# Performance work log

Measured on AMD Instinct MI355X. Metric: run time of the kernel, lower is better.

The kernel has to match this reference:

```python
import jax, jax.numpy as jnp
import numpy as np

TEMP_LEN = 16
TARGET_LEN = 22
DIM = 768
HEADS = 12
B = 16
NT = TEMP_LEN * TEMP_LEN          # 256 template tokens
NG = TARGET_LEN * TARGET_LEN      # 484 target tokens
N = NT + NG                       # 740
POS_HID = 512


def _gaussian_heatmap(center, size, sig=1.0):
    x_axis = np.linspace(0, size[0] - 1, size[0]) - center[0]
    y_axis = np.linspace(0, size[1] - 1, size[1]) - center[1]
    xx, yy = np.meshgrid(x_axis, y_axis)
    return np.exp(-0.5 * (xx ** 2 + yy ** 2) / sig ** 2)


def _bias_index(L):
    # faithful to getBiasIndex (w_len == h_len here)
    coords = np.stack(np.meshgrid(np.arange(L), np.arange(L), indexing='ij'))  # [2,L,L]
    flat = coords.reshape(2, -1)                                               # [2,L*L]
    rel = (flat[:, :, None] - flat[:, None, :]).transpose(1, 2, 0).astype(np.int64)
    rel[:, :, 0] += L - 1
    rel[:, :, 1] += L - 1
    rel[:, :, 0] *= 2 * L - 1
    return rel.sum(-1)  # [L*L, L*L]


def setup_inputs() -> dict:
    key = jax.random.key(0)
    ks = jax.random.split(key, 12)
    f32 = jnp.float32
    x = jax.random.normal(ks[0], (B, N, DIM), dtype=f32)
    temp_q = jax.random.normal(ks[1], (B, NT, DIM), dtype=f32)
    target_q = jax.random.normal(ks[2], (B, NG, DIM), dtype=f32)
    # linear weights stored [in, out] (transposed torch layout)
    w = lambda k, i, o: jax.random.normal(k, (i, o), dtype=f32) * 0.02
    q_w = w(ks[3], DIM, DIM)
    k_w = w(ks[4], DIM, DIM)
    v_w = w(ks[5], DIM, DIM)
    proj_w = w(ks[6], DIM, DIM)
    proj_b = jnp.zeros((DIM,), dtype=f32)
    rpb_table = jax.random.normal(ks[7], ((2 * TARGET_LEN - 1) ** 2, HEADS), dtype=f32) * 0.0002
    rpb_table_temp = jax.random.normal(ks[8], ((2 * TEMP_LEN - 1) ** 2, HEADS), dtype=f32) * 0.0002
    pos_w1 = w(ks[9], 2, POS_HID)
    pos_b1 = jnp.zeros((POS_HID,), dtype=f32)
    pos_w2 = w(ks[10], POS_HID, HEADS)
    pos_b2 = jnp.zeros((HEADS,), dtype=f32)
    # deterministic cross-bias coordinate table (non-learned buffer)
    temp_tab = _gaussian_heatmap((TEMP_LEN // 2, TEMP_LEN // 2), (TEMP_LEN, TEMP_LEN)).astype(np.float32).flatten() \
        + np.linspace(-0.2, 0.2, NT, dtype=np.float32)
    targ_tab = _gaussian_heatmap((TARGET_LEN // 2, TARGET_LEN // 2), (TARGET_LEN, TARGET_LEN)).astype(np.float32).flatten() \
        + np.linspace(-0.2, 0.2, NG, dtype=np.float32)
    # torch.meshgrid default indexing='ij': [2, NT, NG] -> permute(1,2,0) -> [NT,NG,2]
    temp_target = np.stack(np.meshgrid(temp_tab, targ_tab, indexing='ij')).transpose(1, 2, 0)
    target_temp_tab = jnp.asarray(temp_target.transpose(1, 0, 2))  # [NG, NT, 2]
    temp_idx = jnp.asarray(_bias_index(TEMP_LEN))       # [NT, NT] int64
    target_idx = jnp.asarray(_bias_index(TARGET_LEN))   # [NG, NG] int64
    return {
        'x': x, 'temp_q': temp_q, 'target_q': target_q,
        'q_w': q_w, 'k_w': k_w, 'v_w': v_w, 'proj_w': proj_w, 'proj_b': proj_b,
        'rpb_table': rpb_table, 'rpb_table_temp': rpb_table_temp,
        'pos_w1': pos_w1, 'pos_b1': pos_b1, 'pos_w2': pos_w2, 'pos_b2': pos_b2,
        'target_temp_tab': target_temp_tab,
        'temp_idx': temp_idx, 'target_idx': target_idx,
    }


def reference(x, temp_q, target_q, q_w, k_w, v_w, proj_w, proj_b,
              rpb_table, rpb_table_temp, pos_w1, pos_b1, pos_w2, pos_b2,
              target_temp_tab, temp_idx, target_idx):
    Bsz, Ntok, C = x.shape
    H = HEADS
    hd = C // H
    scale = hd ** -0.5

    q_in = jnp.concatenate([temp_q, target_q], axis=1)                 # [B,N,C]
    q = (q_in @ q_w).reshape(Bsz, Ntok, H, hd).transpose(0, 2, 1, 3)   # [B,H,N,hd]
    k = (x @ k_w).reshape(Bsz, Ntok, H, hd).transpose(0, 2, 1, 3)
    v = (x @ v_w).reshape(Bsz, Ntok, H, hd).transpose(0, 2, 1, 3)

    # gathered relative position biases -> [H, Ni, Ni]
    temp_rpb = rpb_table_temp[temp_idx.reshape(-1)].reshape(NT, NT, H).transpose(2, 0, 1)
    targ_rpb = rpb_table[target_idx.reshape(-1)].reshape(NG, NG, H).transpose(2, 0, 1)
    # MLP cross bias: [NG, NT, 2] -> [NG, NT, H] -> [H, NG, NT]
    hid = jax.nn.relu(target_temp_tab @ pos_w1 + pos_b1)
    target_temp_bias = (hid @ pos_w2 + pos_b2).transpose(2, 0, 1)      # [H,NG,NT]
    temp_target_bias = target_temp_bias.transpose(0, 2, 1)             # [H,NT,NG]
    top = jnp.concatenate([temp_rpb, temp_target_bias], axis=2)        # [H,NT,N]
    bot = jnp.concatenate([target_temp_bias, targ_rpb], axis=2)        # [H,NG,N]
    bias = jnp.concatenate([top, bot], axis=1)[None]                   # [1,H,N,N]

    attn = jnp.einsum('bhnd,bhmd->bhnm', q, k) * scale + bias
    attn = jax.nn.softmax(attn, axis=-1)
    out = jnp.einsum('bhnm,bhmd->bhnd', attn, v).transpose(0, 2, 1, 3).reshape(Bsz, Ntok, C)
    return out @ proj_w + proj_b
```

## Files before the change

### kernel.cpp

```cpp
#include <hip/hip_runtime.h>


typedef unsigned short u16;
typedef short bf16x8 __attribute__((ext_vector_type(8)));
typedef float f32x4 __attribute__((ext_vector_type(4)));

#define BSZ   16
#define NTOK  740
#define NTMP  256
#define NTGT  484
#define DIMC  768
#define NHEAD 12
#define HDIM  64
#define MROWS (BSZ*NTOK)
#define LOG2E 1.44269504f
#define NEGS  (-23.0831032f)

__device__ __forceinline__ float bflo(unsigned int u) {
    return __uint_as_float(u << 16);
}
__device__ __forceinline__ float bfhi(unsigned int u) {
    return __uint_as_float(u & 0xffff0000u);
}
__device__ __forceinline__ u16 f2bf(float f) {
    unsigned int u = __float_as_uint(f);
    u += 0x7fffu + ((u >> 16) & 1u);
    return (u16)(u >> 16);
}

__device__ __forceinline__ void gl_lds16(const u16* g, u16* l) {
    __builtin_amdgcn_global_load_lds(
        (const __attribute__((address_space(1))) unsigned int*)(unsigned long long)g,
        (__attribute__((address_space(3))) unsigned int*)(unsigned int)(unsigned long long)l,
        16, 0, 0);
}

__device__ __forceinline__ size_t b2off(int h, int i, int j) {
    return ((size_t)(h * NTOK + i)) * 768 + ((j >> 6) << 6) + ((j & 15) << 2) + ((j >> 4) & 3);
}

#define PREP_MLP  484
#define PREP_TRW  (PREP_MLP + 576)
#define PREP_ALL  (PREP_TRW + 2220)

__global__ __launch_bounds__(256) void prep_kernel(
    const float* __restrict__ w0, const float* __restrict__ w1,
    const float* __restrict__ w2, const float* __restrict__ w3,
    u16* __restrict__ Wt,
    const float* __restrict__ rpb, const float* __restrict__ rpbt,
    const int* __restrict__ tidx, const int* __restrict__ gidx,
    const float* __restrict__ pw1, const float* __restrict__ pb1,
    const float* __restrict__ pw2, const float* __restrict__ pb2,
    const float* __restrict__ tab, u16* __restrict__ bias)
{
    __shared__ float T[64][65];
    const int blk = blockIdx.x;
    const int tid = threadIdx.x;

    if (blk < PREP_MLP) {
        int g = blk;
        int t = tid;
        float a  = tab[(g * NTMP + t) * 2 + 0];
        float bb = tab[(g * NTMP + t) * 2 + 1];
        float acc[NHEAD];
        #pragma unroll
        for (int h = 0; h < NHEAD; h++) acc[h] = pb2[h];
        for (int k = 0; k < 512; k++) {
            float hid = fmaxf(a * pw1[k] + bb * pw1[512 + k] + pb1[k], 0.0f);
            #pragma unroll
            for (int h = 0; h < NHEAD; h++) acc[h] += hid * pw2[k * NHEAD + h];
        }
        #pragma unroll
        for (int h = 0; h < NHEAD; h++) {
            u16 v = f2bf(acc[h] * LOG2E);
            bias[b2off(h, t, NTMP + g)] = v;
            bias[b2off(h, NTMP + g, t)] = v;
        }
    } else if (blk < PREP_TRW) {
        int t = blk - PREP_MLP;
        int z = t / 144, rem = t - z * 144;
        int bx = rem % 12, by = rem / 12;
        const float* src = (z == 0) ? w0 : (z == 1) ? w1 : (z == 2) ? w2 : w3;
        const float scale = (z == 0) ? 0.125f * LOG2E : 1.0f;
        u16* dst = Wt + (size_t)z * DIMC * DIMC;
        int out0 = bx * 64, in0 = by * 64;
        #pragma unroll
        for (int l = 0; l < 4; l++) {
            int u = tid + (l << 8);
            int r = u >> 4, c4 = (u & 15) << 2;
            float4 p = *(const float4*)(src + (size_t)(in0 + r) * DIMC + out0 + c4);
            T[r][c4] = p.x; T[r][c4 + 1] = p.y; T[r][c4 + 2] = p.z; T[r][c4 + 3] = p.w;
        }
        __syncthreads();
        #pragma unroll
        for (int l = 0; l < 2; l++) {
            int u = tid + (l << 8);
            int r = u >> 3, c8 = (u & 7) << 3;
            u16 e[8];
            #pragma unroll
            for (int i = 0; i < 8; i++) e[i] = f2bf(T[c8 + i][r] * scale);
            *(uint4*)(dst + (size_t)(out0 + r) * DIMC + in0 + c8) = *(uint4*)e;
        }
    } else {
        int t = blk - PREP_TRW;
        int jb = t % 3, i = t / 3;
        int j = jb * 256 + tid;
        u16 vals[NHEAD];
        if (j >= NTOK) {
            u16 neg = f2bf(-1e30f);
            #pragma unroll
            for (int h = 0; h < NHEAD; h++) vals[h] = neg;
        } else if (i < NTMP && j < NTMP) {
            int idx = tidx[i * NTMP + j];
            #pragma unroll
            for (int h = 0; h < NHEAD; h++) vals[h] = f2bf(rpbt[idx * NHEAD + h] * LOG2E);
        } else if (i >= NTMP && j >= NTMP) {
            int idx = gidx[(i - NTMP) * NTGT + (j - NTMP)];
            #pragma unroll
            for (int h = 0; h < NHEAD; h++) vals[h] = f2bf(rpb[idx * NHEAD + h] * LOG2E);
        } else {
            return;
        }
        #pragma unroll
        for (int h = 0; h < NHEAD; h++) bias[b2off(h, i, j)] = vals[h];
    }
}

__global__ __launch_bounds__(256, 4) void gemm_qkv(
    const float* __restrict__ x, const float* __restrict__ tq,
    const float* __restrict__ gq, const u16* __restrict__ Wt,
    u16* __restrict__ Qo, u16* __restrict__ Ko, u16* __restrict__ Vo)
{
    __shared__ __align__(16) u16 As[4096];
    __shared__ __align__(16) u16 Bs[2][8192];
    const int tid = threadIdx.x;
    const int lane = tid & 63, w = tid >> 6;
    const int quad = lane >> 4, ln = lane & 15;

    const int nwg = 18 * 185;
    const int flat = blockIdx.y * 18 + blockIdx.x;
    const int q = nwg >> 3, r = nwg & 7;
    const int xcd = flat & 7, sidx = flat >> 3;
    const int wg = (xcd < r) ? xcd * (q + 1) + sidx
                             : r * (q + 1) + (xcd - r) * q + sidx;
    const int by = wg / 18, bx = wg - by * 18;

    const int m0 = by << 6;
    const int wm = (w >> 1) << 5, wn = (w & 1) << 6;

    const int p = (bx < 6) ? 0 : (bx < 12) ? 1 : 2;
    const int nn = (bx - p * 6) << 7;
    const u16* Wb = Wt + (size_t)p * DIMC * DIMC + (size_t)nn * DIMC;
    u16* Co = (p == 0) ? Qo : (p == 1) ? Ko : Vo;

    const int rr = tid >> 2, qq = tid & 3;
    const int arow = m0 + rr;
    const float* aptr;
    if (p == 0) {
        int b = arow / NTOK, n = arow - b * NTOK;
        aptr = (n < NTMP)
             ? tq + ((size_t)(b * NTMP + n)) * DIMC
             : gq + ((size_t)(b * NTGT + (n - NTMP))) * DIMC;
    } else {
        aptr = x + (size_t)arow * DIMC;
    }
    const int wof0 = ((2 * qq + 0) * 64 + (rr ^ (2 * qq + 0))) * 8;
    const int wof1 = ((2 * qq + 1) * 64 + (rr ^ (2 * qq + 1))) * 8;

    float4 a0, a1, a2, a3;

#define LOADA(t) do {                                                         \
    const float* s_ = aptr + ((t) << 6) + (qq << 4);                          \
    a0 = ((const float4*)s_)[0]; a1 = ((const float4*)s_)[1];                 \
    a2 = ((const float4*)s_)[2]; a3 = ((const float4*)s_)[3];                 \
    } while (0)

#define WRITEA() do {                                                         \
    u16 e_[16] = {f2bf(a0.x), f2bf(a0.y), f2bf(a0.z), f2bf(a0.w),             \
                  f2bf(a1.x), f2bf(a1.y), f2bf(a1.z), f2bf(a1.w),             \
                  f2bf(a2.x), f2bf(a2.y), f2bf(a2.z), f2bf(a2.w),             \
                  f2bf(a3.x), f2bf(a3.y), f2bf(a3.z), f2bf(a3.w)};            \
    *(uint4*)&As[wof0] = ((uint4*)e_)[0];                                     \
    *(uint4*)&As[wof1] = ((uint4*)e_)[1];                                     \
    } while (0)

#define STAGEB(t, s) do {                                                     \
    _Pragma("unroll")                                                         \
    for (int l = 0; l < 4; l++) {                                             \
        int f = tid + (l << 8);                                               \
        int c8 = f >> 7, r2 = f & 127;                                        \
        gl_lds16(Wb + (size_t)r2 * DIMC + ((t) << 6) + c8 * 8, &Bs[s][f * 8]); \
    } } while (0)

    f32x4 acc[2][4];
    #pragma unroll
    for (int i = 0; i < 2; i++)
        #pragma unroll
        for (int j = 0; j < 4; j++) acc[i][j] = (f32x4){0.f, 0.f, 0.f, 0.f};

    LOADA(0);
    STAGEB(0, 0);
    __syncthreads();
    WRITEA();
    __syncthreads();

    int buf = 0;
    #pragma unroll 1
    for (int t = 0; t < 12; t++) {
        if (t < 11) {
            LOADA(t + 1);
            STAGEB(t + 1, buf ^ 1);
        }
        #pragma unroll
        for (int kp = 0; kp < 2; kp++) {
            const int kc0 = (kp << 2) + quad;
            bf16x8 af[2], bfr[4];
            #pragma unroll
            for (int mt = 0; mt < 2; mt++)
                af[mt] = *(const bf16x8*)
                    &As[(kc0 * 64 + ((wm + mt * 16 + ln) ^ kc0)) * 8];
            #pragma unroll
            for (int nt = 0; nt < 4; nt++)
                bfr[nt] = *(const bf16x8*)
                    &Bs[buf][(kc0 * 128 + wn + nt * 16 + ln) * 8];
            #pragma unroll
            for (int mt = 0; mt < 2; mt++)
                #pragma unroll
                for (int nt = 0; nt < 4; nt++)
                    acc[mt][nt] = __builtin_amdgcn_mfma_f32_16x16x32_bf16(
                        af[mt], bfr[nt], acc[mt][nt], 0, 0, 0);
        }
        if (t < 11) {
            __syncthreads();
            WRITEA();
            __syncthreads();
            buf ^= 1;
        }
    }
#undef LOADA
#undef WRITEA
#undef STAGEB

    #pragma unroll
    for (int mt = 0; mt < 2; mt++)
        #pragma unroll
        for (int reg = 0; reg < 4; reg++) {
            int grow = m0 + wm + mt * 16 + (quad << 2) + reg;
            #pragma unroll
            for (int nt = 0; nt < 4; nt++)
                Co[(size_t)grow * DIMC + nn + wn + nt * 16 + ln]
                    = f2bf(acc[mt][nt][reg]);
        }
}

__global__ __launch_bounds__(256) void gemm_proj(
    const u16* __restrict__ A, const u16* __restrict__ Wt,
    const float* __restrict__ pb, float* __restrict__ Cf)
{
    __shared__ __align__(16) u16 As[2][8192];
    __shared__ __align__(16) u16 Bs[2][8192];
    const int tid = threadIdx.x;
    const int lane = tid & 63, w = tid >> 6;
    const int quad = lane >> 4, ln = lane & 15;

    const int nwg = 6 * 93;
    const int flat = blockIdx.y * 6 + blockIdx.x;
    const int q = nwg >> 3, r = nwg & 7;
    const int xcd = flat & 7, sidx = flat >> 3;
    const int wg = (xcd < r) ? xcd * (q + 1) + sidx
                             : r * (q + 1) + (xcd - r) * q + sidx;
    const int by = wg / 6, bx = wg - by * 6;

    const int m0 = by << 7;
    const int wm = (w >> 1) << 6, wn = (w & 1) << 6;
    const int nn = bx << 7;
    const u16* Wb = Wt + (size_t)nn * DIMC;

    f32x4 acc[4][4];
    #pragma unroll
    for (int i = 0; i < 4; i++)
        #pragma unroll
        for (int j = 0; j < 4; j++)
            acc[i][j] = (f32x4){0.f, 0.f, 0.f, 0.f};

#define STAGE(s, k0) do {                                                     \
    _Pragma("unroll")                                                         \
    for (int l = 0; l < 4; l++) {                                             \
        int f = tid + (l << 8);                                  \
        int c8 = f >> 7, rr = f & 127;                                        \
        int grow = m0 + rr; if (grow >= MROWS) grow = MROWS - 1;              \
        gl_lds16(A + (size_t)grow * DIMC + (k0) + c8 * 8, &As[s][f * 8]);     \
        gl_lds16(Wb + (size_t)rr * DIMC + (k0) + c8 * 8, &Bs[s][f * 8]);      \
    } } while (0)

#define COMPUTE(s) do {                                                       \
    _Pragma("unroll")                                                         \
    for (int kp = 0; kp < 2; kp++) {                                          \
        bf16x8 af[4], bfr[4];                                                 \
        _Pragma("unroll")                                                     \
        for (int mt = 0; mt < 4; mt++)                                        \
            af[mt] = *(const bf16x8*)                                         \
                &As[s][(((kp << 2) + quad) * 128 + wm + mt * 16 + ln) * 8];   \
        _Pragma("unroll")                                                     \
        for (int nt = 0; nt < 4; nt++)                                        \
            bfr[nt] = *(const bf16x8*)                                        \
                &Bs[s][(((kp << 2) + quad) * 128 + wn + nt * 16 + ln) * 8];   \
        _Pragma("unroll")                                                     \
        for (int mt = 0; mt < 4; mt++)                                        \
            _Pragma("unroll")                                                 \
            for (int nt = 0; nt < 4; nt++)                                    \
                acc[mt][nt] = __builtin_amdgcn_mfma_f32_16x16x32_bf16(        \
                    af[mt], bfr[nt], acc[mt][nt], 0, 0, 0);                   \
    } } while (0)

    STAGE(0, 0);
    __syncthreads();
    #pragma unroll 1
    for (int t = 0; t < 12; t += 2) {
        STAGE(1, (t + 1) << 6);
        COMPUTE(0);
        __syncthreads();
        if (t < 10) STAGE(0, (t + 2) << 6);
        COMPUTE(1);
        __syncthreads();
    }

#undef STAGE
#undef COMPUTE

    #pragma unroll
    for (int mt = 0; mt < 4; mt++) {
        #pragma unroll
        for (int reg = 0; reg < 4; reg++) {
            int grow = m0 + wm + mt * 16 + (quad << 2) + reg;
            if (grow >= MROWS) continue;
            #pragma unroll
            for (int nt = 0; nt < 4; nt++) {
                int gcol = nn + wn + nt * 16 + ln;
                Cf[(size_t)grow * DIMC + gcol] = acc[mt][nt][reg] + pb[gcol];
            }
        }
    }
}

__global__ __launch_bounds__(256) void attn_mfma(
    const u16* __restrict__ Qg, const u16* __restrict__ Kg,
    const u16* __restrict__ Vg, const u16* __restrict__ bias,
    u16* __restrict__ ctx)
{
    __shared__ __align__(16) u16 KsL[4096];
    __shared__ __align__(16) u16 VtL[64 * 72];
    __shared__ __align__(16) u16 Pw[4][16][72];

    const int tid = threadIdx.x;
    const int lane = tid & 63, w = tid >> 6;
    const int quad = lane >> 4, ln = lane & 15;

    const int flat = (blockIdx.z * 12 + blockIdx.y) * 12 + blockIdx.x;
    const int wg = (flat & 7) * 288 + (flat >> 3);
    const int h = wg / 192;
    const int rem = wg - h * 192;
    const int b = rem / 12;
    const int q0 = (rem - b * 12) << 6;

    const int mbase = q0 + (w << 4);
    const u16* bp = bias + ((size_t)h * NTOK) * 768;

    bf16x8 aq[2];
    {
        int qrow = mbase + ln; if (qrow >= NTOK) qrow = NTOK - 1;
        #pragma unroll
        for (int kp = 0; kp < 2; kp++)
            aq[kp] = *(const bf16x8*)(Qg + ((size_t)(b * NTOK + qrow)) * DIMC
                                      + h * HDIM + kp * 32 + (quad << 3));
    }
    int boff[4];
    #pragma unroll
    for (int reg = 0; reg < 4; reg++) {
        int rr = mbase + (quad << 2) + reg;
        if (rr >= NTOK) rr = NTOK - 1;
        boff[reg] = rr * 768 + (ln << 2);
    }

    const int pswz = ((ln >> 2) & 3) << 4;

    float rs[4] = {};
    f32x4 O[4];
    #pragma unroll
    for (int dt = 0; dt < 4; dt++) O[dt] = (f32x4){0.f, 0.f, 0.f, 0.f};

    for (int j0 = 0; j0 < NTOK; j0 += 64) {
        __syncthreads();
        #pragma unroll
        for (int l = 0; l < 2; l++) {
            int f = tid + (l << 8);
            int chunk = f >> 6, jr = f & 63;
            int krow = j0 + jr; if (krow >= NTOK) krow = NTOK - 1;
            gl_lds16(Kg + ((size_t)(b * NTOK + krow)) * DIMC + h * HDIM + chunk * 8,
                     KsL + f * 8);
        }
        uint2 bvv[4];
        #pragma unroll
        for (int reg = 0; reg < 4; reg++)
            bvv[reg] = *(const uint2*)(bp + boff[reg] + j0);
        #pragma unroll
        for (int l = 0; l < 2; l++) {
            int u = tid + (l << 8);
            int jr = u >> 3, d0 = (u & 7) << 3;
            int vrow = j0 + jr; if (vrow >= NTOK) vrow = NTOK - 1;
            uint4 p = *(const uint4*)(Vg + ((size_t)(b * NTOK + vrow)) * DIMC + h * HDIM + d0);
            const u16* pe = (const u16*)&p;
            int jswz = jr ^ d0;
            #pragma unroll
            for (int i = 0; i < 8; i++) VtL[(d0 + i) * 72 + jswz] = pe[i];
        }
        __syncthreads();

        bf16x8 bv[4][2];
        #pragma unroll
        for (int dt = 0; dt < 4; dt++) {
            int key8 = ((dt * 2 + (ln >> 3)) & 7) << 3;
            #pragma unroll
            for (int kp = 0; kp < 2; kp++) {
                int koff = (kp * 32 + (quad << 3)) ^ key8;
                bv[dt][kp] = *(const bf16x8*)&VtL[(dt * 16 + ln) * 72 + koff];
            }
        }

        f32x4 s[4];
        #pragma unroll
        for (int nt = 0; nt < 4; nt++) s[nt] = (f32x4){NEGS, NEGS, NEGS, NEGS};
        __builtin_amdgcn_s_setprio(1);
        #pragma unroll
        for (int kp = 0; kp < 2; kp++)
            #pragma unroll
            for (int nt = 0; nt < 4; nt++) {
                bf16x8 bk = *(const bf16x8*)
                    &KsL[(((kp << 2) + quad) * 64 + nt * 16 + ln) * 8];
                s[nt] = __builtin_amdgcn_mfma_f32_16x16x32_bf16(aq[kp], bk, s[nt], 0, 0, 0);
            }
        __builtin_amdgcn_s_setprio(0);

        #pragma unroll
        for (int reg = 0; reg < 4; reg++) {
            uint2 bb = bvv[reg];
            float p0 = __builtin_exp2f(s[0][reg] + bflo(bb.x));
            float p1 = __builtin_exp2f(s[1][reg] + bfhi(bb.x));
            float p2 = __builtin_exp2f(s[2][reg] + bflo(bb.y));
            float p3 = __builtin_exp2f(s[3][reg] + bfhi(bb.y));
            s[0][reg] = p0; s[1][reg] = p1;
            s[2][reg] = p2; s[3][reg] = p3;
            rs[reg] += p0 + p1 + p2 + p3;
        }
        u16* pwb = &Pw[w][0][0];
        #pragma unroll
        for (int nt = 0; nt < 4; nt++) {
            int colw = ((nt ^ quad) << 4) + ln;
            #pragma unroll
            for (int reg = 0; reg < 4; reg++)
                pwb[((quad << 2) + reg) * 72 + colw] = f2bf(s[nt][reg]);
        }
        bf16x8 ap[2];
        #pragma unroll
        for (int kp = 0; kp < 2; kp++) {
            int koff = (kp * 32 + (quad << 3)) ^ pswz;
            ap[kp] = *(const bf16x8*)&pwb[ln * 72 + koff];
        }
        __builtin_amdgcn_s_setprio(1);
        #pragma unroll
        for (int dt = 0; dt < 4; dt++)
            #pragma unroll
            for (int kp = 0; kp < 2; kp++)
                O[dt] = __builtin_amdgcn_mfma_f32_16x16x32_bf16(
                    ap[kp], bv[dt][kp], O[dt], 0, 0, 0);
        __builtin_amdgcn_s_setprio(0);
    }

    #pragma unroll
    for (int reg = 0; reg < 4; reg++) {
        float t = rs[reg];
        #pragma unroll
        for (int mk = 8; mk >= 1; mk >>= 1) t += __shfl_xor(t, mk);
        float inv = 1.0f / t;
        int row = mbase + (quad << 2) + reg;
        if (row < NTOK) {
            #pragma unroll
            for (int dt = 0; dt < 4; dt++)
                ctx[((size_t)(b * NTOK + row)) * DIMC + h * HDIM + dt * 16 + ln]
                    = f2bf(O[dt][reg] * inv);
        }
    }
}

extern "C" void kernel_launch(void* const* d_in, const int* in_sizes, int n_in,
                              void* d_out, int out_size, void* d_ws, size_t ws_size,
                              hipStream_t stream)
{
    const float* x        = (const float*)d_in[0];
    const float* temp_q   = (const float*)d_in[1];
    const float* target_q = (const float*)d_in[2];
    const float* q_w      = (const float*)d_in[3];
    const float* k_w      = (const float*)d_in[4];
    const float* v_w      = (const float*)d_in[5];
    const float* proj_w   = (const float*)d_in[6];
    const float* proj_b   = (const float*)d_in[7];
    const float* rpb      = (const float*)d_in[8];
    const float* rpbt     = (const float*)d_in[9];
    const float* pw1      = (const float*)d_in[10];
    const float* pb1      = (const float*)d_in[11];
    const float* pw2      = (const float*)d_in[12];
    const float* pb2      = (const float*)d_in[13];
    const float* tab      = (const float*)d_in[14];
    const int*   tidx     = (const int*)d_in[15];
    const int*   gidx     = (const int*)d_in[16];
    float* out = (float*)d_out;

    char* ws = (char*)d_ws;
    const size_t S = (size_t)MROWS * DIMC * sizeof(u16);
    const size_t SZB = (size_t)NHEAD * NTOK * 768 * sizeof(u16);
    u16* CTX   = (u16*)(ws);
    u16* V     = (u16*)(ws + S);
    u16* Q     = (u16*)(ws + 2 * S);
    u16* K     = (u16*)(ws + 3 * S);
    u16* BIAS2 = (u16*)(ws + 4 * S);
    u16* WT    = (u16*)(ws + 4 * S + SZB);

    prep_kernel<<<dim3(PREP_ALL), 256, 0, stream>>>(
        q_w, k_w, v_w, proj_w, WT,
        rpb, rpbt, tidx, gidx,
        pw1, pb1, pw2, pb2, tab, BIAS2);

    const u16* WTp = WT + 3 * (size_t)DIMC * DIMC;

    gemm_qkv<<<dim3(18, 185), 256, 0, stream>>>(x, temp_q, target_q, WT, Q, K, V);
    attn_mfma<<<dim3(12, 12, 16), 256, 0, stream>>>(Q, K, V, BIAS2, CTX);
    gemm_proj<<<dim3(6, 93), 256, 0, stream>>>(CTX, WTp, proj_b, out);
}
```

Baseline: 472.8 us.

## Pre-convert x to bf16 once and stage K/V GEMM A-tiles via direct LDS loads

Adds a prep-kernel section that converts x to bf16 once into a workspace buffer that is later reused for the attention context. The K and V projection blocks now load their A tiles with global_load_lds double buffering instead of loading fp32 per tile, converting in registers and writing to LDS. The aim is to avoid converting x twice (once for K, once for V) and to cut the fp32 read traffic and the extra LDS writes and barriers in the GEMM. In exchange the prep kernel writes and re-reads an extra bf16 copy of x, shared memory per block grows, and the occupancy hint drops from 4 to 3 blocks.

Measured after the change: 465.3 us. No clear change (-1.6%).

```diff
diff --git a/kernel.cpp b/kernel.cpp
--- a/kernel.cpp
+++ b/kernel.cpp
@@ -40,10 +40,12 @@
 }
 
 #define PREP_MLP  484
-#define PREP_TRW  (PREP_MLP + 576)
+#define PREP_CONV (PREP_MLP + 2220)
+#define PREP_TRW  (PREP_CONV + 576)
 #define PREP_ALL  (PREP_TRW + 2220)
 
 __global__ __launch_bounds__(256) void prep_kernel(
+    const float* __restrict__ x, u16* __restrict__ XB,
     const float* __restrict__ w0, const float* __restrict__ w1,
     const float* __restrict__ w2, const float* __restrict__ w3,
     u16* __restrict__ Wt,
@@ -76,8 +78,25 @@
             bias[b2off(h, t, NTMP + g)] = v;
             bias[b2off(h, NTMP + g, t)] = v;
         }
+    } else if (blk < PREP_CONV) {
+        int t0 = (blk - PREP_MLP) * 512 + tid;
+        int t1 = t0 + 256;
+        const float* s0 = x + (size_t)t0 * 8;
+        const float* s1 = x + (size_t)t1 * 8;
+        float4 a0 = ((const float4*)s0)[0], a1 = ((const float4*)s0)[1];
+        float4 b0 = ((const float4*)s1)[0], b1 = ((const float4*)s1)[1];
+        {
+            u16 e[8] = {f2bf(a0.x), f2bf(a0.y), f2bf(a0.z), f2bf(a0.w),
+                        f2bf(a1.x), f2bf(a1.y), f2bf(a1.z), f2bf(a1.w)};
+            *(uint4*)(XB + (size_t)t0 * 8) = *(uint4*)e;
+        }
+        {
+            u16 e[8] = {f2bf(b0.x), f2bf(b0.y), f2bf(b0.z), f2bf(b0.w),
+                        f2bf(b1.x), f2bf(b1.y), f2bf(b1.z), f2bf(b1.w)};
+            *(uint4*)(XB + (size_t)t1 * 8) = *(uint4*)e;
+        }
     } else if (blk < PREP_TRW) {
-        int t = blk - PREP_MLP;
+        int t = blk - PREP_CONV;
         int z = t / 144, rem = t - z * 144;
         int bx = rem % 12, by = rem / 12;
         const float* src = (z == 0) ? w0 : (z == 1) ? w1 : (z == 2) ? w2 : w3;
@@ -126,13 +145,12 @@
     }
 }
 
-__global__ __launch_bounds__(256, 4) void gemm_qkv(
-    const float* __restrict__ x, const float* __restrict__ tq,
-    const float* __restrict__ gq, const u16* __restrict__ Wt,
+__global__ __launch_bounds__(256, 3) void gemm_qkv(
+    const float* __restrict__ tq, const float* __restrict__ gq,
+    const u16* __restrict__ XB, const u16* __restrict__ Wt,
     u16* __restrict__ Qo, u16* __restrict__ Ko, u16* __restrict__ Vo)
 {
-    __shared__ __align__(16) u16 As[4096];
-    __shared__ __align__(16) u16 Bs[2][8192];
+    __shared__ __align__(16) u16 SH[2][12288];
     const int tid = threadIdx.x;
     const int lane = tid & 63, w = tid >> 6;
     const int quad = lane >> 4, ln = lane & 15;
@@ -153,21 +171,32 @@
     const u16* Wb = Wt + (size_t)p * DIMC * DIMC + (size_t)nn * DIMC;
     u16* Co = (p == 0) ? Qo : (p == 1) ? Ko : Vo;
 
-    const int rr = tid >> 2, qq = tid & 3;
-    const int arow = m0 + rr;
-    const float* aptr;
+#define BS(s) (&SH[s][4096])
+#define STAGEB(t, s) do {                                                     \
+    _Pragma("unroll")                                                         \
+    for (int l = 0; l < 4; l++) {                                             \
+        int f = tid + (l << 8);                                               \
+        int c8 = f >> 7, r2 = f & 127;                                        \
+        gl_lds16(Wb + (size_t)r2 * DIMC + ((t) << 6) + c8 * 8, BS(s) + f * 8); \
+    } } while (0)
+
+    f32x4 acc[2][4];
+    #pragma unroll
+    for (int i = 0; i < 2; i++)
+        #pragma unroll
+        for (int j = 0; j < 4; j++) acc[i][j] = (f32x4){0.f, 0.f, 0.f, 0.f};
+
     if (p == 0) {
+        u16* Asq = &SH[0][0];
+        const int rr = tid >> 2, qq = tid & 3;
+        const int arow = m0 + rr;
         int b = arow / NTOK, n = arow - b * NTOK;
-        aptr = (n < NTMP)
-             ? tq + ((size_t)(b * NTMP + n)) * DIMC
-             : gq + ((size_t)(b * NTGT + (n - NTMP))) * DIMC;
-    } else {
-        aptr = x + (size_t)arow * DIMC;
-    }
-    const int wof0 = ((2 * qq + 0) * 64 + (rr ^ (2 * qq + 0))) * 8;
-    const int wof1 = ((2 * qq + 1) * 64 + (rr ^ (2 * qq + 1))) * 8;
-
-    float4 a0, a1, a2, a3;
+        const float* aptr = (n < NTMP)
+                          ? tq + ((size_t)(b * NTMP + n)) * DIMC
+                          : gq + ((size_t)(b * NTGT + (n - NTMP))) * DIMC;
+        const int wof0 = ((2 * qq + 0) * 64 + (rr ^ (2 * qq + 0))) * 8;
+        const int wof1 = ((2 * qq + 1) * 64 + (rr ^ (2 * qq + 1))) * 8;
+        float4 a0, a1, a2, a3;
 
 #define LOADA(t) do {                                                         \
     const float* s_ = aptr + ((t) << 6) + (qq << 4);                          \
@@ -180,65 +209,100 @@
                   f2bf(a1.x), f2bf(a1.y), f2bf(a1.z), f2bf(a1.w),             \
                   f2bf(a2.x), f2bf(a2.y), f2bf(a2.z), f2bf(a2.w),             \
                   f2bf(a3.x), f2bf(a3.y), f2bf(a3.z), f2bf(a3.w)};            \
-    *(uint4*)&As[wof0] = ((uint4*)e_)[0];                                     \
-    *(uint4*)&As[wof1] = ((uint4*)e_)[1];                                     \
+    *(uint4*)&Asq[wof0] = ((uint4*)e_)[0];                                    \
+    *(uint4*)&Asq[wof1] = ((uint4*)e_)[1];                                    \
     } while (0)
 
-#define STAGEB(t, s) do {                                                     \
-    _Pragma("unroll")                                                         \
-    for (int l = 0; l < 4; l++) {                                             \
-        int f = tid + (l << 8);                                               \
-        int c8 = f >> 7, r2 = f & 127;                                        \
-        gl_lds16(Wb + (size_t)r2 * DIMC + ((t) << 6) + c8 * 8, &Bs[s][f * 8]); \
-    } } while (0)
-
-    f32x4 acc[2][4];
-    #pragma unroll
-    for (int i = 0; i < 2; i++)
-        #pragma unroll
-        for (int j = 0; j < 4; j++) acc[i][j] = (f32x4){0.f, 0.f, 0.f, 0.f};
-
-    LOADA(0);
-    STAGEB(0, 0);
-    __syncthreads();
-    WRITEA();
-    __syncthreads();
-
-    int buf = 0;
-    #pragma unroll 1
-    for (int t = 0; t < 12; t++) {
-        if (t < 11) {
-            LOADA(t + 1);
-            STAGEB(t + 1, buf ^ 1);
-        }
-        #pragma unroll
-        for (int kp = 0; kp < 2; kp++) {
-            const int kc0 = (kp << 2) + quad;
-            bf16x8 af[2], bfr[4];
-            #pragma unroll
-            for (int mt = 0; mt < 2; mt++)
-                af[mt] = *(const bf16x8*)
-                    &As[(kc0 * 64 + ((wm + mt * 16 + ln) ^ kc0)) * 8];
-            #pragma unroll
-            for (int nt = 0; nt < 4; nt++)
-                bfr[nt] = *(const bf16x8*)
-                    &Bs[buf][(kc0 * 128 + wn + nt * 16 + ln) * 8];
-            #pragma unroll
-            for (int mt = 0; mt < 2; mt++)
+        LOADA(0);
+        STAGEB(0, 0);
+        __syncthreads();
+        WRITEA();
+        __syncthreads();
+
+        int buf = 0;
+        #pragma unroll 1
+        for (int t = 0; t < 12; t++) {
+            if (t < 11) {
+                LOADA(t + 1);
+                STAGEB(t + 1, buf ^ 1);
+            }
+            #pragma unroll
+            for (int kp = 0; kp < 2; kp++) {
+                const int kc0 = (kp << 2) + quad;
+                bf16x8 af[2], bfr[4];
+                #pragma unroll
+                for (int mt = 0; mt < 2; mt++)
+                    af[mt] = *(const bf16x8*)
+                        &Asq[(kc0 * 64 + ((wm + mt * 16 + ln) ^ kc0)) * 8];
                 #pragma unroll
                 for (int nt = 0; nt < 4; nt++)
-                    acc[mt][nt] = __builtin_amdgcn_mfma_f32_16x16x32_bf16(
-                        af[mt], bfr[nt], acc[mt][nt], 0, 0, 0);
-        }
-        if (t < 11) {
-            __syncthreads();
-            WRITEA();
+                    bfr[nt] = *(const bf16x8*)
+                        &BS(buf)[(kc0 * 128 + wn + nt * 16 + ln) * 8];
+                #pragma unroll
+                for (int mt = 0; mt < 2; mt++)
+                    #pragma unroll
+                    for (int nt = 0; nt < 4; nt++)
+                        acc[mt][nt] = __builtin_amdgcn_mfma_f32_16x16x32_bf16(
+                            af[mt], bfr[nt], acc[mt][nt], 0, 0, 0);
+            }
+            if (t < 11) {
+                __syncthreads();
+                WRITEA();
+                __syncthreads();
+                buf ^= 1;
+            }
+        }
+#undef LOADA
+#undef WRITEA
+    } else {
+        const u16* Ab = XB + (size_t)m0 * DIMC;
+
+#define ASK(s) (&SH[s][0])
+#define STAGEA(t, s) do {                                                     \
+    _Pragma("unroll")                                                         \
+    for (int l = 0; l < 2; l++) {                                             \
+        int f = tid + (l << 8);                                               \
+        int c8 = f >> 6, r2 = f & 63;                                         \
+        gl_lds16(Ab + (size_t)r2 * DIMC + ((t) << 6) + c8 * 8, ASK(s) + f * 8); \
+    } } while (0)
+
+        STAGEA(0, 0);
+        STAGEB(0, 0);
+        __syncthreads();
+
+        int buf = 0;
+        #pragma unroll 1
+        for (int t = 0; t < 12; t++) {
+            if (t < 11) {
+                STAGEA(t + 1, buf ^ 1);
+                STAGEB(t + 1, buf ^ 1);
+            }
+            #pragma unroll
+            for (int kp = 0; kp < 2; kp++) {
+                const int kc0 = (kp << 2) + quad;
+                bf16x8 af[2], bfr[4];
+                #pragma unroll
+                for (int mt = 0; mt < 2; mt++)
+                    af[mt] = *(const bf16x8*)
+                        &ASK(buf)[(kc0 * 64 + wm + mt * 16 + ln) * 8];
+                #pragma unroll
+                for (int nt = 0; nt < 4; nt++)
+                    bfr[nt] = *(const bf16x8*)
+                        &BS(buf)[(kc0 * 128 + wn + nt * 16 + ln) * 8];
+                #pragma unroll
+                for (int mt = 0; mt < 2; mt++)
+                    #pragma unroll
+                    for (int nt = 0; nt < 4; nt++)
+                        acc[mt][nt] = __builtin_amdgcn_mfma_f32_16x16x32_bf16(
+                            af[mt], bfr[nt], acc[mt][nt], 0, 0, 0);
+            }
             __syncthreads();
             buf ^= 1;
         }
-    }
-#undef LOADA
-#undef WRITEA
+#undef ASK
+#undef STAGEA
+    }
+#undef BS
 #undef STAGEB
 
     #pragma unroll
@@ -518,21 +582,22 @@
     char* ws = (char*)d_ws;
     const size_t S = (size_t)MROWS * DIMC * sizeof(u16);
     const size_t SZB = (size_t)NHEAD * NTOK * 768 * sizeof(u16);
-    u16* CTX   = (u16*)(ws);
+    u16* XB    = (u16*)(ws);
     u16* V     = (u16*)(ws + S);
     u16* Q     = (u16*)(ws + 2 * S);
     u16* K     = (u16*)(ws + 3 * S);
+    u16* CTX   = XB;
     u16* BIAS2 = (u16*)(ws + 4 * S);
     u16* WT    = (u16*)(ws + 4 * S + SZB);
 
     prep_kernel<<<dim3(PREP_ALL), 256, 0, stream>>>(
-        q_w, k_w, v_w, proj_w, WT,
+        x, XB, q_w, k_w, v_w, proj_w, WT,
         rpb, rpbt, tidx, gidx,
         pw1, pb1, pw2, pb2, tab, BIAS2);
 
     const u16* WTp = WT + 3 * (size_t)DIMC * DIMC;
 
-    gemm_qkv<<<dim3(18, 185), 256, 0, stream>>>(x, temp_q, target_q, WT, Q, K, V);
+    gemm_qkv<<<dim3(18, 185), 256, 0, stream>>>(temp_q, target_q, XB, WT, Q, K, V);
     attn_mfma<<<dim3(12, 12, 16), 256, 0, stream>>>(Q, K, V, BIAS2, CTX);
     gemm_proj<<<dim3(6, 93), 256, 0, stream>>>(CTX, WTp, proj_b, out);
 }
```
